# Performance work log

Hardware: AMD Instinct MI355X
Metric: run time of the kernel (lower is better)

The kernel has to match this reference:

```python
import jax, jax.numpy as jnp
import numpy as np

N_SUB, N_AGR, N_URB = 200000, 400000, 200000
H, OUT = 64, 6
E_SS, E_AS, E_US = 2000000, 4000000, 2000000
NLAYERS = 3


def setup_inputs() -> dict:
    key = jax.random.key(0)
    ks = jax.random.split(key, 12)
    s = 0.05
    return {
        "x_sub": jax.random.normal(ks[0], (N_SUB, H), jnp.float32),
        "x_agr": jax.random.normal(ks[1], (N_AGR, H), jnp.float32),
        "x_urb": jax.random.normal(ks[2], (N_URB, H), jnp.float32),
        # stacked SAGEConv params: [layer, relation(ss,as,us), ...]
        "Wl": jax.random.normal(ks[3], (NLAYERS, 3, H, H), jnp.float32) * s,
        "bl": jax.random.normal(ks[4], (NLAYERS, 3, H), jnp.float32) * s,
        "Wr": jax.random.normal(ks[5], (NLAYERS, 3, H, H), jnp.float32) * s,
        "Wf": jax.random.normal(ks[6], (OUT, H), jnp.float32) * s,
        "bf": jnp.zeros((OUT,), jnp.float32),
        "edge_ss": jax.random.randint(ks[7], (2, E_SS), 0, N_SUB, jnp.int32),
        "edge_as_src": jax.random.randint(ks[8], (E_AS,), 0, N_AGR, jnp.int32),
        "edge_as_dst": jax.random.randint(ks[9], (E_AS,), 0, N_SUB, jnp.int32),
        "edge_us": jax.random.randint(ks[10], (2, E_US), 0, N_SUB, jnp.int32),
    }


def _sage(x_src, x_dst, src, dst, Wl, b, Wr, n_dst, mean):
    # PyG SAGEConv: lin_l(aggr_j x_j) + lin_r(x_i); lin_r has no bias
    msg = x_src[src]                                   # [E, d_src] gather
    agg = jax.ops.segment_sum(msg, dst, num_segments=n_dst)
    if mean:  # static python flag
        deg = jax.ops.segment_sum(jnp.ones((src.shape[0], 1), x_src.dtype),
                                  dst, num_segments=n_dst)
        agg = agg / jnp.maximum(deg, 1.0)
    return agg @ Wl.T + b + x_dst @ Wr.T


def reference(x_sub, x_agr, x_urb, Wl, bl, Wr, Wf, bf,
              edge_ss, edge_as_src, edge_as_dst, edge_us):
    sub = x_sub
    for i in range(NLAYERS):
        mean_ss = i > 0  # layer-0 sub->sub uses aggr='sum', later layers PyG default 'mean'
        h = _sage(sub, sub, edge_ss[0], edge_ss[1], Wl[i, 0], bl[i, 0], Wr[i, 0], N_SUB, mean_ss)
        h = h + _sage(x_agr, sub, edge_as_src, edge_as_dst, Wl[i, 1], bl[i, 1], Wr[i, 1], N_SUB, False)
        h = h + _sage(x_urb, sub, edge_us[0], edge_us[1], Wl[i, 2], bl[i, 2], Wr[i, 2], N_SUB, False)
        sub = jax.nn.relu(h)  # Identity norm (batch_norm=False), dropout is eval-mode identity
        # x_dict['agr'] / x_dict['urb'] reset to skip features -> agr/urb convs never affect output
    return jax.nn.softmax(sub @ Wf.T + bf, axis=1)
```

## Files before the change

### kernel.cpp

```cpp
#include <hip/hip_runtime.h>
#include <cstdio>
#include <cstdint>


#define NSUB 200000
#define NAGR 400000
#define NURB 200000
#define HDIM 64
#define ESS 2000000
#define EAS 4000000
#define EUS 2000000
#define NB 512
#define CAP_AS 8608
#define CAP_SS 4320
#define CAP_US 4320
#define CHUNK 4096
#define NCH_AS 977
#define NCH_SS 489
#define NCH_US 489
#define COL_SLACK 16384
#define CDIV(a,b) (((a)+(b)-1)/(b))

using u16 = unsigned short;
typedef __attribute__((ext_vector_type(8))) short v8s;
typedef __attribute__((ext_vector_type(4))) float v4f;
typedef __attribute__((ext_vector_type(2))) float v2f;
typedef __attribute__((ext_vector_type(4))) unsigned int v4u;

__device__ __forceinline__ float bu2f(u16 u){
  union { unsigned int i; float f; } c; c.i = ((unsigned int)u) << 16; return c.f;
}
__device__ __forceinline__ u16 f2bu(float x){
  union { float f; unsigned int i; } c; c.f = x;
  unsigned int r = c.i + 0x7fffu + ((c.i >> 16) & 1u);
  return (u16)(r >> 16);
}
__device__ __forceinline__ int bucket_of(int d){
  return (int)(((unsigned long long)(unsigned)d * NB) / NSUB);
}
__device__ __forceinline__ int bucket_base(int b){
  return (int)(((unsigned long long)b * NSUB + NB - 1) / NB);
}

__global__ void kcast(const float4* __restrict__ in, uint2* __restrict__ outp, int n4){
  int i = blockIdx.x*256 + threadIdx.x;
  if(i<n4){
    float4 v = in[i];
    uint2 o;
    o.x = (unsigned int)f2bu(v.x) | ((unsigned int)f2bu(v.y)<<16);
    o.y = (unsigned int)f2bu(v.z) | ((unsigned int)f2bu(v.w)<<16);
    outp[i]=o;
  }
}

__global__ void kcast2(const float4* __restrict__ a, uint2* __restrict__ oa, int n4a,
                       const float4* __restrict__ u, uint2* __restrict__ ou, int n4u){
  int i = blockIdx.x*256 + threadIdx.x;
  if(i < n4a){
    float4 v = a[i];
    uint2 o;
    o.x = (unsigned int)f2bu(v.x) | ((unsigned int)f2bu(v.y)<<16);
    o.y = (unsigned int)f2bu(v.z) | ((unsigned int)f2bu(v.w)<<16);
    oa[i]=o;
  } else if(i < n4a + n4u){
    int idx = i - n4a;
    float4 v = u[idx];
    uint2 o;
    o.x = (unsigned int)f2bu(v.x) | ((unsigned int)f2bu(v.y)<<16);
    o.y = (unsigned int)f2bu(v.z) | ((unsigned int)f2bu(v.w)<<16);
    ou[idx]=o;
  } else {
    int k = i - n4a - n4u;
    uint2 z; z.x=0u; z.y=0u;
    if(k < 16) oa[(size_t)n4a + k] = z;
    else if(k < 32) ou[(size_t)n4u + (k-16)] = z;
  }
}

__global__ void kprep(const float* __restrict__ Wl, const float* __restrict__ Wr,
                      const float* __restrict__ bl, u16* __restrict__ Wg,
                      float* __restrict__ bsum, int* __restrict__ gcur,
                      u16* __restrict__ zA, u16* __restrict__ zB){
  int l = blockIdx.x, tid = threadIdx.x;
  for(int i=tid; i<16384; i+=256){
    int o = i>>8, k = i&255, a = k>>6, kk = k&63;
    float v;
    if(a<3) v = Wl[(((size_t)l*3+a)*64+o)*64+kk];
    else    v = Wr[(((size_t)l*3+0)*64+o)*64+kk]
              + Wr[(((size_t)l*3+1)*64+o)*64+kk]
              + Wr[(((size_t)l*3+2)*64+o)*64+kk];
    Wg[((size_t)l*64+o)*256 + k] = f2bu(v);
  }
  if(tid<64) bsum[l*64+tid] = bl[(l*3+0)*64+tid] + bl[(l*3+1)*64+tid] + bl[(l*3+2)*64+tid];
  for(int i=tid;i<NB;i+=256) gcur[l*NB+i]=0;
  if(l==0){
    uint2 z; z.x=0u; z.y=0u;
    if(tid<16)          ((uint2*)(zA + (size_t)NSUB*HDIM))[tid]    = z;
    else if(tid<32)     ((uint2*)(zB + (size_t)NSUB*HDIM))[tid-16] = z;
  }
}

__global__ __launch_bounds__(256) void kpart(
    const int* __restrict__ e_ss, const int* __restrict__ e_as_s,
    const int* __restrict__ e_as_d, const int* __restrict__ e_us,
    unsigned* __restrict__ pAS, unsigned* __restrict__ pSS,
    unsigned* __restrict__ pUS, int* __restrict__ gcur){
  __shared__ int cnt[NB];
  __shared__ int seg[NB];
  int bid = blockIdx.x, tid = threadIdx.x;
  int rel, chunk, cap, Erel;
  const int *sp, *dp; unsigned* part;
  if(bid < NCH_AS){ rel=0; chunk=bid; sp=e_as_s; dp=e_as_d; part=pAS; cap=CAP_AS; Erel=EAS; }
  else if(bid < NCH_AS+NCH_SS){ rel=1; chunk=bid-NCH_AS; sp=e_ss; dp=e_ss+ESS; part=pSS; cap=CAP_SS; Erel=ESS; }
  else { rel=2; chunk=bid-NCH_AS-NCH_SS; sp=e_us; dp=e_us+EUS; part=pUS; cap=CAP_US; Erel=EUS; }
  int m = Erel - chunk*CHUNK; if(m>CHUNK) m=CHUNK;
  for(int i=tid;i<NB;i+=256) cnt[i]=0;
  __syncthreads();
  unsigned pk[16], meta[16];
  #pragma unroll
  for(int j=0;j<16;j++){
    int idx = j*256+tid;
    meta[j] = 0xFFFFFFFFu;
    if(idx < m){
      long i = (long)chunk*CHUNK + idx;
      int s = sp[i], d = dp[i];
      int b = bucket_of(d);
      int r = atomicAdd(&cnt[b],1);
      pk[j] = ((unsigned)s<<9) | (unsigned)(d - bucket_base(b));
      meta[j] = ((unsigned)b<<16) | (unsigned)r;
    }
  }
  __syncthreads();
  for(int q=tid;q<NB;q+=256){
    int c = cnt[q];
    seg[q] = c ? atomicAdd(&gcur[rel*NB+q], c) : 0;
  }
  __syncthreads();
  #pragma unroll
  for(int j=0;j<16;j++){
    if(meta[j]!=0xFFFFFFFFu){
      int b = meta[j]>>16, r = meta[j]&0xFFFF;
      int pos = seg[b] + r;
      if(pos < cap) part[(long)b*cap + pos] = pk[j];
    }
  }
}

__global__ void kbscan(const int* __restrict__ gcur, int* __restrict__ boff){
  __shared__ int s1[256];
  int t = threadIdx.x;
  for(int rel=0; rel<3; rel++){
    int cap = (rel==0)?CAP_AS:((rel==1)?CAP_SS:CAP_US);
    int g0 = gcur[rel*NB + 2*t], g1 = gcur[rel*NB + 2*t+1];
    int a0 = g0<cap?g0:cap, a1 = g1<cap?g1:cap;
    s1[t] = a0+a1;
    __syncthreads();
    for(int off=1; off<256; off<<=1){
      int x = s1[t];
      int y = (t>=off)?s1[t-off]:0;
      __syncthreads();
      s1[t] = x+y;
      __syncthreads();
    }
    int e2 = s1[t]-(a0+a1);
    boff[rel*NB + 2*t]   = e2;
    boff[rel*NB + 2*t+1] = e2+a0;
    __syncthreads();
  }
}

__global__ __launch_bounds__(256) void ksort(
    const unsigned* __restrict__ pAS, const unsigned* __restrict__ pSS,
    const unsigned* __restrict__ pUS, const int* __restrict__ gcur,
    const int* __restrict__ boff,
    int* __restrict__ colAS, int* __restrict__ colSS, int* __restrict__ colUS,
    int* __restrict__ rpAS, int* __restrict__ rpSS, int* __restrict__ rpUS,
    int* __restrict__ degAS, int* __restrict__ degSS, int* __restrict__ degUS){
  __shared__ int degl[512];
  __shared__ int excl[512];
  __shared__ int cur[512];
  __shared__ int s1[256];
  int bid = blockIdx.x;
  int rel = bid >> 9, b = bid & 511;
  const unsigned* part; int cap; int* col; int* rp; int* deg;
  if(rel==0){ part=pAS; cap=CAP_AS; col=colAS; rp=rpAS; deg=degAS; }
  else if(rel==1){ part=pSS; cap=CAP_SS; col=colSS; rp=rpSS; deg=degSS; }
  else { part=pUS; cap=CAP_US; col=colUS; rp=rpUS; deg=degUS; }
  int tid = threadIdx.x;
  int base_b = bucket_base(b);
  int base_n = (b+1==NB)?NSUB:bucket_base(b+1);
  int width = base_n - base_b;
  int size = gcur[rel*NB+b]; if(size>cap) size=cap;
  int bo = boff[rel*NB+b];
  const unsigned* pb = part + (long)b*cap;
  degl[tid]=0; degl[256+tid]=0;
  __syncthreads();
  for(int i=tid;i<size;i+=256) atomicAdd(&degl[pb[i]&511u],1);
  __syncthreads();
  int a0=degl[2*tid], a1=degl[2*tid+1];
  s1[tid]=a0+a1;
  __syncthreads();
  for(int off=1; off<256; off<<=1){
    int x=s1[tid];
    int y=(tid>=off)?s1[tid-off]:0;
    __syncthreads();
    s1[tid]=x+y;
    __syncthreads();
  }
  int e2 = s1[tid]-(a0+a1);
  excl[2*tid]=e2;     excl[2*tid+1]=e2+a0;
  cur[2*tid]=e2;      cur[2*tid+1]=e2+a0;
  __syncthreads();
  for(int n=tid;n<width;n+=256){
    rp[base_b+n]  = bo + excl[n];
    deg[base_b+n] = degl[n];
  }
  for(int i=tid;i<size;i+=256){
    unsigned p = pb[i];
    int dl = (int)(p&511u);
    int r = atomicAdd(&cur[dl],1);
    col[bo + r] = (int)(p>>9);
  }
}

__device__ __forceinline__ float gather1(const float* x, size_t idx){ return x[idx]; }

template<bool MEAN>
__device__ __forceinline__ void agg_one_f32(const float* __restrict__ x,
    const int* __restrict__ rowptr, const int* __restrict__ deg,
    const int* __restrict__ col, u16* __restrict__ out, int w, int lane){
  int s = __builtin_amdgcn_readfirstlane(rowptr[w]);
  int d = __builtin_amdgcn_readfirstlane(deg[w]);
  float acc = 0.f;
  int i=0;
  for(; i+8<=d; i+=8){
    int sj[8];
    #pragma unroll
    for(int j=0;j<8;j++) sj[j]=col[s+i+j];
    float a[8];
    #pragma unroll
    for(int j=0;j<8;j++) a[j]=gather1(x,(size_t)sj[j]*HDIM+lane);
    acc += ((a[0]+a[1])+(a[2]+a[3])) + ((a[4]+a[5])+(a[6]+a[7]));
  }
  for(; i<d; i++) acc += gather1(x,(size_t)col[s+i]*HDIM+lane);
  float sc = 1.f;
  if(MEAN) sc = 1.f/(float)(d>1?d:1);
  out[(size_t)w*HDIM + lane] = f2bu(acc*sc);
}

__global__ __launch_bounds__(256) void kaggAUf(
    const float* __restrict__ xa, const int* __restrict__ rpA,
    const int* __restrict__ degA, const int* __restrict__ colA,
    u16* __restrict__ outA,
    const float* __restrict__ xu, const int* __restrict__ rpU,
    const int* __restrict__ degU, const int* __restrict__ colU,
    u16* __restrict__ outU){
  int gid = blockIdx.x*256 + threadIdx.x;
  int w = gid>>6, lane = gid&63;
  if(w < NSUB)        agg_one_f32<false>(xa, rpA, degA, colA, outA, w, lane);
  else if(w < 2*NSUB) agg_one_f32<false>(xu, rpU, degU, colU, outU, w-NSUB, lane);
}

template<bool MEAN>
__device__ __forceinline__ void agg_pair(const u16* __restrict__ x,
    const int* __restrict__ rowptr, const int* __restrict__ deg,
    const int* __restrict__ col, u16* __restrict__ out,
    int w0, int lane, int zrow){
  int h  = lane>>5;
  int gl = (lane>>3)&3;
  int q  = lane&7;
  int w  = w0 + h;
  int s  = rowptr[w];
  int d  = deg[w];
  int d0 = __builtin_amdgcn_readlane(d, 0);
  int d1 = __builtin_amdgcn_readlane(d, 32);
  int dm = d0 > d1 ? d0 : d1;
  const u16* xq = x + ((unsigned)q<<3);
  v2f acc[4];
  #pragma unroll
  for(int k=0;k<4;k++){ acc[k].x=0.f; acc[k].y=0.f; }
  for(int i=0; i<dm; i+=16){
    int eb = i + gl;
    const int* cp = col + (s + eb);
    int cj[4];
    #pragma unroll
    for(int j=0;j<4;j++){
      int c = cp[j*4];
      cj[j] = (eb + j*4 < d) ? c : zrow;
    }
    v8s vv[4];
    #pragma unroll
    for(int j=0;j<4;j++)
      vv[j] = *(const v8s*)(xq + (size_t)(unsigned)cj[j]*HDIM);
    #pragma unroll
    for(int j=0;j<4;j++){
      v4u dw = __builtin_bit_cast(v4u, vv[j]);
      #pragma unroll
      for(int k=0;k<4;k++){
        unsigned v = dw[k];
        v2f p;
        p.x = __uint_as_float(v << 16);
        p.y = __uint_as_float(v & 0xffff0000u);
        acc[k] += p;
      }
    }
  }
  #pragma unroll
  for(int k=0;k<4;k++){
    v2f v = acc[k];
    v2f t;
    t.x = __shfl_xor(v.x, 8);  t.y = __shfl_xor(v.y, 8);  v += t;
    t.x = __shfl_xor(v.x, 16); t.y = __shfl_xor(v.y, 16); v += t;
    acc[k] = v;
  }
  float sc = 1.f;
  if(MEAN) sc = 1.f/(float)(d>1?d:1);
  if(gl==0){
    v4u r;
    #pragma unroll
    for(int k=0;k<4;k++)
      r[k] = (unsigned)f2bu(acc[k].x*sc) | ((unsigned)f2bu(acc[k].y*sc)<<16);
    *(v4u*)(out + (size_t)w*HDIM + ((unsigned)q<<3)) = r;
  }
}

template<bool MEAN>
__global__ __launch_bounds__(256) void kaggP(
    const u16* __restrict__ x, const int* __restrict__ rowptr,
    const int* __restrict__ deg, const int* __restrict__ col,
    u16* __restrict__ out, int npair, int zrow){
  int gid = blockIdx.x*256 + threadIdx.x;
  int p = gid>>6, lane = gid&63;
  if(p>=npair) return;
  agg_pair<MEAN>(x, rowptr, deg, col, out, 2*p, lane, zrow);
}

__global__ __launch_bounds__(256) void kaggAUP(
    const u16* __restrict__ xa, const int* __restrict__ rpA,
    const int* __restrict__ degA, const int* __restrict__ colA,
    u16* __restrict__ outA,
    const u16* __restrict__ xu, const int* __restrict__ rpU,
    const int* __restrict__ degU, const int* __restrict__ colU,
    u16* __restrict__ outU){
  int gid = blockIdx.x*256 + threadIdx.x;
  int p = gid>>6, lane = gid&63;
  if(p < NSUB/2)      agg_pair<false>(xa, rpA, degA, colA, outA, 2*p, lane, NAGR);
  else if(p < NSUB)   agg_pair<false>(xu, rpU, degU, colU, outU, 2*(p-NSUB/2), lane, NURB);
}

__global__ __launch_bounds__(256) void kgemmM(
    const u16* __restrict__ aggSS, const u16* __restrict__ aggAS,
    const u16* __restrict__ aggUS, const u16* __restrict__ subIn,
    const u16* __restrict__ Wg, const float* __restrict__ bsum,
    u16* __restrict__ subOut){
  __shared__ u16 ldsW[64*264];
  __shared__ float ldsB[64];
  int tid = threadIdx.x;
  const unsigned* wg32 = (const unsigned*)Wg;
  for(int i=tid; i<8192; i+=256){
    int o = i>>7, k2 = i&127;
    ((unsigned*)ldsW)[o*132 + k2] = wg32[i];
  }
  if(tid<64) ldsB[tid] = bsum[tid];
  __syncthreads();
  int lane = tid&63, wid = tid>>6;
  long row0 = (long)blockIdx.x*64 + wid*16;
  const u16* arrs[4] = {aggSS, aggAS, aggUS, subIn};
  v4f acc[4] = {};
  long rowl = row0 + (lane&15);
  int kq = (lane>>4)*8;
  #pragma unroll
  for(int s=0;s<8;s++){
    const u16* ap = arrs[s>>1] + rowl*64 + (s&1)*32 + kq;
    v8s a = *(const v8s*)ap;
    #pragma unroll
    for(int t=0;t<4;t++){
      v8s bf = *(const v8s*)&ldsW[(t*16+(lane&15))*264 + s*32 + kq];
      acc[t] = __builtin_amdgcn_mfma_f32_16x16x32_bf16(a, bf, acc[t], 0,0,0);
    }
  }
  int m0 = (lane>>4)*4;
  #pragma unroll
  for(int t=0;t<4;t++){
    int o = t*16 + (lane&15);
    float bb = ldsB[o];
    #pragma unroll
    for(int r=0;r<4;r++){
      float h = acc[t][r] + bb;
      h = fmaxf(h, 0.f);
      subOut[(row0 + m0 + r)*64 + o] = f2bu(h);
    }
  }
}

__global__ void khead(const u16* __restrict__ sub, const float* __restrict__ Wf,
                      const float* __restrict__ bfv, float* __restrict__ out, int n){
  __shared__ float w[6*64];
  __shared__ float b[6];
  for(int j=threadIdx.x; j<384; j+=256) w[j]=Wf[j];
  if(threadIdx.x<6) b[threadIdx.x]=bfv[threadIdx.x];
  __syncthreads();
  int i = blockIdx.x*256 + threadIdx.x;
  if(i>=n) return;
  const unsigned int* row = (const unsigned int*)(sub + (size_t)i*HDIM);
  float d0=b[0],d1=b[1],d2=b[2],d3=b[3],d4=b[4],d5=b[5];
  #pragma unroll 8
  for(int k2=0;k2<32;k2++){
    unsigned int v = row[k2];
    float lo = bu2f((u16)(v&0xffffu));
    float hi = bu2f((u16)(v>>16));
    int k = 2*k2;
    d0 += lo*w[0*64+k] + hi*w[0*64+k+1];
    d1 += lo*w[1*64+k] + hi*w[1*64+k+1];
    d2 += lo*w[2*64+k] + hi*w[2*64+k+1];
    d3 += lo*w[3*64+k] + hi*w[3*64+k+1];
    d4 += lo*w[4*64+k] + hi*w[4*64+k+1];
    d5 += lo*w[5*64+k] + hi*w[5*64+k+1];
  }
  float m = fmaxf(fmaxf(fmaxf(d0,d1),fmaxf(d2,d3)),fmaxf(d4,d5));
  float e0=expf(d0-m), e1=expf(d1-m), e2=expf(d2-m);
  float e3=expf(d3-m), e4=expf(d4-m), e5=expf(d5-m);
  float inv = 1.0f/(e0+e1+e2+e3+e4+e5);
  float2* op = (float2*)(out + (size_t)i*6);
  float2 r0; r0.x=e0*inv; r0.y=e1*inv;
  float2 r1; r1.x=e2*inv; r1.y=e3*inv;
  float2 r2; r2.x=e4*inv; r2.y=e5*inv;
  op[0]=r0; op[1]=r1; op[2]=r2;
}

extern "C" void kernel_launch(void* const* d_in, const int* in_sizes, int n_in,
                              void* d_out, int out_size, void* d_ws, size_t ws_size,
                              hipStream_t stream) {
  const float* x_sub = (const float*)d_in[0];
  const float* x_agr = (const float*)d_in[1];
  const float* x_urb = (const float*)d_in[2];
  const float* Wl    = (const float*)d_in[3];
  const float* bl    = (const float*)d_in[4];
  const float* Wr    = (const float*)d_in[5];
  const float* Wf    = (const float*)d_in[6];
  const float* bfv   = (const float*)d_in[7];
  const int* e_ss    = (const int*)d_in[8];
  const int* e_as_s  = (const int*)d_in[9];
  const int* e_as_d  = (const int*)d_in[10];
  const int* e_us    = (const int*)d_in[11];
  float* out = (float*)d_out;

  char* ws = (char*)d_ws;
  size_t off = 0;
  auto alloc = [&](size_t bytes)->void*{
    void* p = ws + off; off += (bytes + 255) & ~(size_t)255; return p;
  };
  u16*  subA   = (u16*) alloc((size_t)(NSUB+1)*HDIM*2);
  u16*  subB   = (u16*) alloc((size_t)(NSUB+1)*HDIM*2);
  u16*  aggSS  = (u16*) alloc((size_t)NSUB*HDIM*2);
  u16*  aggAS  = (u16*) alloc((size_t)NSUB*HDIM*2);
  u16*  aggUS  = (u16*) alloc((size_t)NSUB*HDIM*2);
  int*  colAS  = (int*)  alloc((size_t)(EAS+COL_SLACK)*4);
  int*  colSS  = (int*)  alloc((size_t)(ESS+COL_SLACK)*4);
  int*  colUS  = (int*)  alloc((size_t)(EUS+COL_SLACK)*4);
  int*  rpAS   = (int*)  alloc((size_t)NSUB*4);
  int*  rpSS   = (int*)  alloc((size_t)NSUB*4);
  int*  rpUS   = (int*)  alloc((size_t)NSUB*4);
  int*  degAS  = (int*)  alloc((size_t)NSUB*4);
  int*  degSS  = (int*)  alloc((size_t)NSUB*4);
  int*  degUS  = (int*)  alloc((size_t)NSUB*4);
  int*  gcur   = (int*)  alloc((size_t)3*NB*4);
  int*  boff   = (int*)  alloc((size_t)3*NB*4);
  u16*  Wg     = (u16*)  alloc((size_t)3*64*256*2);
  float* bsum  = (float*)alloc((size_t)3*64*4);
  size_t off0 = off;
  unsigned* pAS = (unsigned*)alloc((size_t)NB*CAP_AS*4);
  unsigned* pSS = (unsigned*)alloc((size_t)NB*CAP_SS*4);
  unsigned* pUS = (unsigned*)alloc((size_t)NB*CAP_US*4);
  size_t end_part = off;
  u16* agr16 = (u16*)(ws + off0);
  u16* urb16 = agr16 + (size_t)(NAGR+1)*HDIM;
  size_t end_cast = off0 + ((size_t)NAGR+NURB+2)*HDIM*2;
  size_t need_full = end_part > end_cast ? end_part : end_cast;
  bool bf16_gather = (ws_size >= need_full);
  if(ws_size < end_part){
    fprintf(stderr, "kernel_launch: ws too small: need %zu have %zu\n", end_part, ws_size);
    return;
  }

  kcast<<<CDIV(NSUB*HDIM/4,256),256,0,stream>>>((const float4*)x_sub, (uint2*)subA, NSUB*HDIM/4);
  kprep<<<3,256,0,stream>>>(Wl, Wr, bl, Wg, bsum, gcur, subA, subB);

  kpart<<<NCH_AS+NCH_SS+NCH_US,256,0,stream>>>(e_ss, e_as_s, e_as_d, e_us,
                                               pAS, pSS, pUS, gcur);
  kbscan<<<1,256,0,stream>>>(gcur, boff);
  ksort<<<3*NB,256,0,stream>>>(pAS, pSS, pUS, gcur, boff,
                               colAS, colSS, colUS,
                               rpAS, rpSS, rpUS,
                               degAS, degSS, degUS);

  if(bf16_gather){
    int n4a = NAGR*HDIM/4, n4u = NURB*HDIM/4;
    kcast2<<<CDIV(n4a+n4u+32,256),256,0,stream>>>((const float4*)x_agr, (uint2*)agr16, n4a,
                                                  (const float4*)x_urb, (uint2*)urb16, n4u);
    kaggAUP<<<NSUB*64/256,256,0,stream>>>(agr16, rpAS, degAS, colAS, aggAS,
                                          urb16, rpUS, degUS, colUS, aggUS);
  } else {
    kaggAUf<<<CDIV(2*NSUB*64,256),256,0,stream>>>(x_agr, rpAS, degAS, colAS, aggAS,
                                                  x_urb, rpUS, degUS, colUS, aggUS);
  }

  const int pairBlocks = (NSUB/2)*64/256;
  const int gemmBlocks = NSUB/64;
  kaggP<false><<<pairBlocks,256,0,stream>>>(subA, rpSS, degSS, colSS, aggSS, NSUB/2, NSUB);
  kgemmM<<<gemmBlocks,256,0,stream>>>(aggSS, aggAS, aggUS, subA, Wg + 0*16384, bsum + 0*64, subB);
  kaggP<true><<<pairBlocks,256,0,stream>>>(subB, rpSS, degSS, colSS, aggSS, NSUB/2, NSUB);
  kgemmM<<<gemmBlocks,256,0,stream>>>(aggSS, aggAS, aggUS, subB, Wg + 1*16384, bsum + 1*64, subA);
  kaggP<true><<<pairBlocks,256,0,stream>>>(subA, rpSS, degSS, colSS, aggSS, NSUB/2, NSUB);
  kgemmM<<<gemmBlocks,256,0,stream>>>(aggSS, aggAS, aggUS, subA, Wg + 2*16384, bsum + 2*64, subB);

  khead<<<CDIV(NSUB,256),256,0,stream>>>(subB, Wf, bfv, out, NSUB);
}
```

Before: 756.8 us.

## Pad CSR rows to multiples of four, pack rowptr/deg, vectorize column loads

```diff
diff --git a/kernel.cpp b/kernel.cpp
--- a/kernel.cpp
+++ b/kernel.cpp
@@ -18,7 +18,7 @@
 #define NCH_AS 977
 #define NCH_SS 489
 #define NCH_US 489
-#define COL_SLACK 16384
+#define COL_PAD (4*NSUB + 256)
 #define CDIV(a,b) (((a)+(b)-1)/(b))
 
 using u16 = unsigned short;
@@ -151,8 +151,11 @@
   int t = threadIdx.x;
   for(int rel=0; rel<3; rel++){
     int cap = (rel==0)?CAP_AS:((rel==1)?CAP_SS:CAP_US);
-    int g0 = gcur[rel*NB + 2*t], g1 = gcur[rel*NB + 2*t+1];
-    int a0 = g0<cap?g0:cap, a1 = g1<cap?g1:cap;
+    int n0 = 2*t, n1 = 2*t+1;
+    int w0 = bucket_base(n0+1) - bucket_base(n0);
+    int w1 = bucket_base(n1+1) - bucket_base(n1);
+    int g0 = gcur[rel*NB + n0], g1 = gcur[rel*NB + n1];
+    int a0 = (g0<cap?g0:cap) + 4*w0, a1 = (g1<cap?g1:cap) + 4*w1;
     s1[t] = a0+a1;
     __syncthreads();
     for(int off=1; off<256; off<<=1){
@@ -163,8 +166,8 @@
       __syncthreads();
     }
     int e2 = s1[t]-(a0+a1);
-    boff[rel*NB + 2*t]   = e2;
-    boff[rel*NB + 2*t+1] = e2+a0;
+    boff[rel*NB + n0] = e2;
+    boff[rel*NB + n1] = e2+a0;
     __syncthreads();
   }
 }
@@ -174,18 +177,17 @@
     const unsigned* __restrict__ pUS, const int* __restrict__ gcur,
     const int* __restrict__ boff,
     int* __restrict__ colAS, int* __restrict__ colSS, int* __restrict__ colUS,
-    int* __restrict__ rpAS, int* __restrict__ rpSS, int* __restrict__ rpUS,
-    int* __restrict__ degAS, int* __restrict__ degSS, int* __restrict__ degUS){
+    int2* __restrict__ rpdAS, int2* __restrict__ rpdSS, int2* __restrict__ rpdUS){
   __shared__ int degl[512];
   __shared__ int excl[512];
   __shared__ int cur[512];
   __shared__ int s1[256];
   int bid = blockIdx.x;
   int rel = bid >> 9, b = bid & 511;
-  const unsigned* part; int cap; int* col; int* rp; int* deg;
-  if(rel==0){ part=pAS; cap=CAP_AS; col=colAS; rp=rpAS; deg=degAS; }
-  else if(rel==1){ part=pSS; cap=CAP_SS; col=colSS; rp=rpSS; deg=degSS; }
-  else { part=pUS; cap=CAP_US; col=colUS; rp=rpUS; deg=degUS; }
+  const unsigned* part; int cap; int* col; int2* rpd;
+  if(rel==0){ part=pAS; cap=CAP_AS; col=colAS; rpd=rpdAS; }
+  else if(rel==1){ part=pSS; cap=CAP_SS; col=colSS; rpd=rpdSS; }
+  else { part=pUS; cap=CAP_US; col=colUS; rpd=rpdUS; }
   int tid = threadIdx.x;
   int base_b = bucket_base(b);
   int base_n = (b+1==NB)?NSUB:bucket_base(b+1);
@@ -197,7 +199,7 @@
   __syncthreads();
   for(int i=tid;i<size;i+=256) atomicAdd(&degl[pb[i]&511u],1);
   __syncthreads();
-  int a0=degl[2*tid], a1=degl[2*tid+1];
+  int a0=(degl[2*tid]+3)&~3, a1=(degl[2*tid+1]+3)&~3;
   s1[tid]=a0+a1;
   __syncthreads();
   for(int off=1; off<256; off<<=1){
@@ -212,8 +214,8 @@
   cur[2*tid]=e2;      cur[2*tid+1]=e2+a0;
   __syncthreads();
   for(int n=tid;n<width;n+=256){
-    rp[base_b+n]  = bo + excl[n];
-    deg[base_b+n] = degl[n];
+    int2 v; v.x = bo + excl[n]; v.y = degl[n];
+    rpd[base_b+n] = v;
   }
   for(int i=tid;i<size;i+=256){
     unsigned p = pb[i];
@@ -223,14 +225,13 @@
   }
 }
 
-__device__ __forceinline__ float gather1(const float* x, size_t idx){ return x[idx]; }
-
 template<bool MEAN>
 __device__ __forceinline__ void agg_one_f32(const float* __restrict__ x,
-    const int* __restrict__ rowptr, const int* __restrict__ deg,
+    const int2* __restrict__ rpd,
     const int* __restrict__ col, u16* __restrict__ out, int w, int lane){
-  int s = __builtin_amdgcn_readfirstlane(rowptr[w]);
-  int d = __builtin_amdgcn_readfirstlane(deg[w]);
+  int2 rd = rpd[w];
+  int s = __builtin_amdgcn_readfirstlane(rd.x);
+  int d = __builtin_amdgcn_readfirstlane(rd.y);
   float acc = 0.f;
   int i=0;
   for(; i+8<=d; i+=8){
@@ -239,39 +240,49 @@
     for(int j=0;j<8;j++) sj[j]=col[s+i+j];
     float a[8];
     #pragma unroll
-    for(int j=0;j<8;j++) a[j]=gather1(x,(size_t)sj[j]*HDIM+lane);
+    for(int j=0;j<8;j++) a[j]=x[(size_t)sj[j]*HDIM+lane];
     acc += ((a[0]+a[1])+(a[2]+a[3])) + ((a[4]+a[5])+(a[6]+a[7]));
   }
-  for(; i<d; i++) acc += gather1(x,(size_t)col[s+i]*HDIM+lane);
+  for(; i<d; i++) acc += x[(size_t)col[s+i]*HDIM+lane];
   float sc = 1.f;
   if(MEAN) sc = 1.f/(float)(d>1?d:1);
   out[(size_t)w*HDIM + lane] = f2bu(acc*sc);
 }
 
 __global__ __launch_bounds__(256) void kaggAUf(
-    const float* __restrict__ xa, const int* __restrict__ rpA,
-    const int* __restrict__ degA, const int* __restrict__ colA,
-    u16* __restrict__ outA,
-    const float* __restrict__ xu, const int* __restrict__ rpU,
-    const int* __restrict__ degU, const int* __restrict__ colU,
-    u16* __restrict__ outU){
+    const float* __restrict__ xa, const int2* __restrict__ rpdA,
+    const int* __restrict__ colA, u16* __restrict__ outA,
+    const float* __restrict__ xu, const int2* __restrict__ rpdU,
+    const int* __restrict__ colU, u16* __restrict__ outU){
   int gid = blockIdx.x*256 + threadIdx.x;
   int w = gid>>6, lane = gid&63;
-  if(w < NSUB)        agg_one_f32<false>(xa, rpA, degA, colA, outA, w, lane);
-  else if(w < 2*NSUB) agg_one_f32<false>(xu, rpU, degU, colU, outU, w-NSUB, lane);
+  if(w < NSUB)        agg_one_f32<false>(xa, rpdA, colA, outA, w, lane);
+  else if(w < 2*NSUB) agg_one_f32<false>(xu, rpdU, colU, outU, w-NSUB, lane);
+}
+
+__device__ __forceinline__ void unpack_acc(v8s vvj, v2f acc[4]){
+  v4u dw = __builtin_bit_cast(v4u, vvj);
+  #pragma unroll
+  for(int k=0;k<4;k++){
+    unsigned v = dw[k];
+    v2f p;
+    p.x = __uint_as_float(v << 16);
+    p.y = __uint_as_float(v & 0xffff0000u);
+    acc[k] += p;
+  }
 }
 
 template<bool MEAN>
 __device__ __forceinline__ void agg_pair(const u16* __restrict__ x,
-    const int* __restrict__ rowptr, const int* __restrict__ deg,
+    const int2* __restrict__ rpd,
     const int* __restrict__ col, u16* __restrict__ out,
     int w0, int lane, int zrow){
   int h  = lane>>5;
   int gl = (lane>>3)&3;
   int q  = lane&7;
   int w  = w0 + h;
-  int s  = rowptr[w];
-  int d  = deg[w];
+  int2 rd = rpd[w];
+  int s = rd.x, d = rd.y;
   int d0 = __builtin_amdgcn_readlane(d, 0);
   int d1 = __builtin_amdgcn_readlane(d, 32);
   int dm = d0 > d1 ? d0 : d1;
@@ -279,30 +290,34 @@
   v2f acc[4];
   #pragma unroll
   for(int k=0;k<4;k++){ acc[k].x=0.f; acc[k].y=0.f; }
-  for(int i=0; i<dm; i+=16){
-    int eb = i + gl;
-    const int* cp = col + (s + eb);
-    int cj[4];
-    #pragma unroll
-    for(int j=0;j<4;j++){
-      int c = cp[j*4];
-      cj[j] = (eb + j*4 < d) ? c : zrow;
-    }
+  if(dm <= 16){
+    const int4 c4 = *(const int4*)(col + s + 4*gl);
+    int cj[4] = {c4.x, c4.y, c4.z, c4.w};
+    #pragma unroll
+    for(int j=0;j<4;j++) cj[j] = (4*gl + j < d) ? cj[j] : zrow;
     v8s vv[4];
     #pragma unroll
     for(int j=0;j<4;j++)
       vv[j] = *(const v8s*)(xq + (size_t)(unsigned)cj[j]*HDIM);
     #pragma unroll
-    for(int j=0;j<4;j++){
-      v4u dw = __builtin_bit_cast(v4u, vv[j]);
+    for(int j=0;j<4;j++) unpack_acc(vv[j], acc);
+  } else {
+    for(int i=0; i<dm; i+=32){
+      const int4 cA = *(const int4*)(col + s + i + 4*gl);
+      const int4 cB = *(const int4*)(col + s + i + 16 + 4*gl);
+      int cj[8] = {cA.x,cA.y,cA.z,cA.w, cB.x,cB.y,cB.z,cB.w};
+      int eb = i + 4*gl;
       #pragma unroll
-      for(int k=0;k<4;k++){
-        unsigned v = dw[k];
-        v2f p;
-        p.x = __uint_as_float(v << 16);
-        p.y = __uint_as_float(v & 0xffff0000u);
-        acc[k] += p;
+      for(int j=0;j<8;j++){
+        int e = eb + (j&3) + ((j>>2)<<4);
+        cj[j] = (e < d) ? cj[j] : zrow;
       }
+      v8s vv[8];
+      #pragma unroll
+      for(int j=0;j<8;j++)
+        vv[j] = *(const v8s*)(xq + (size_t)(unsigned)cj[j]*HDIM);
+      #pragma unroll
+      for(int j=0;j<8;j++) unpack_acc(vv[j], acc);
     }
   }
   #pragma unroll
@@ -326,26 +341,24 @@
 
 template<bool MEAN>
 __global__ __launch_bounds__(256) void kaggP(
-    const u16* __restrict__ x, const int* __restrict__ rowptr,
-    const int* __restrict__ deg, const int* __restrict__ col,
+    const u16* __restrict__ x, const int2* __restrict__ rpd,
+    const int* __restrict__ col,
     u16* __restrict__ out, int npair, int zrow){
   int gid = blockIdx.x*256 + threadIdx.x;
   int p = gid>>6, lane = gid&63;
   if(p>=npair) return;
-  agg_pair<MEAN>(x, rowptr, deg, col, out, 2*p, lane, zrow);
+  agg_pair<MEAN>(x, rpd, col, out, 2*p, lane, zrow);
 }
 
 __global__ __launch_bounds__(256) void kaggAUP(
-    const u16* __restrict__ xa, const int* __restrict__ rpA,
-    const int* __restrict__ degA, const int* __restrict__ colA,
-    u16* __restrict__ outA,
-    const u16* __restrict__ xu, const int* __restrict__ rpU,
-    const int* __restrict__ degU, const int* __restrict__ colU,
-    u16* __restrict__ outU){
+    const u16* __restrict__ xa, const int2* __restrict__ rpdA,
+    const int* __restrict__ colA, u16* __restrict__ outA,
+    const u16* __restrict__ xu, const int2* __restrict__ rpdU,
+    const int* __restrict__ colU, u16* __restrict__ outU){
   int gid = blockIdx.x*256 + threadIdx.x;
   int p = gid>>6, lane = gid&63;
-  if(p < NSUB/2)      agg_pair<false>(xa, rpA, degA, colA, outA, 2*p, lane, NAGR);
-  else if(p < NSUB)   agg_pair<false>(xu, rpU, degU, colU, outU, 2*(p-NSUB/2), lane, NURB);
+  if(p < NSUB/2)      agg_pair<false>(xa, rpdA, colA, outA, 2*p, lane, NAGR);
+  else if(p < NSUB)   agg_pair<false>(xu, rpdU, colU, outU, 2*(p-NSUB/2), lane, NURB);
 }
 
 __global__ __launch_bounds__(256) void kgemmM(
@@ -455,15 +468,12 @@
   u16*  aggSS  = (u16*) alloc((size_t)NSUB*HDIM*2);
   u16*  aggAS  = (u16*) alloc((size_t)NSUB*HDIM*2);
   u16*  aggUS  = (u16*) alloc((size_t)NSUB*HDIM*2);
-  int*  colAS  = (int*)  alloc((size_t)(EAS+COL_SLACK)*4);
-  int*  colSS  = (int*)  alloc((size_t)(ESS+COL_SLACK)*4);
-  int*  colUS  = (int*)  alloc((size_t)(EUS+COL_SLACK)*4);
-  int*  rpAS   = (int*)  alloc((size_t)NSUB*4);
-  int*  rpSS   = (int*)  alloc((size_t)NSUB*4);
-  int*  rpUS   = (int*)  alloc((size_t)NSUB*4);
-  int*  degAS  = (int*)  alloc((size_t)NSUB*4);
-  int*  degSS  = (int*)  alloc((size_t)NSUB*4);
-  int*  degUS  = (int*)  alloc((size_t)NSUB*4);
+  int*  colAS  = (int*)  alloc((size_t)(EAS+COL_PAD)*4);
+  int*  colSS  = (int*)  alloc((size_t)(ESS+COL_PAD)*4);
+  int*  colUS  = (int*)  alloc((size_t)(EUS+COL_PAD)*4);
+  int2* rpdAS  = (int2*) alloc((size_t)NSUB*8);
+  int2* rpdSS  = (int2*) alloc((size_t)NSUB*8);
+  int2* rpdUS  = (int2*) alloc((size_t)NSUB*8);
   int*  gcur   = (int*)  alloc((size_t)3*NB*4);
   int*  boff   = (int*)  alloc((size_t)3*NB*4);
   u16*  Wg     = (u16*)  alloc((size_t)3*64*256*2);
@@ -491,27 +501,26 @@
   kbscan<<<1,256,0,stream>>>(gcur, boff);
   ksort<<<3*NB,256,0,stream>>>(pAS, pSS, pUS, gcur, boff,
                                colAS, colSS, colUS,
-                               rpAS, rpSS, rpUS,
-                               degAS, degSS, degUS);
+                               rpdAS, rpdSS, rpdUS);
 
   if(bf16_gather){
     int n4a = NAGR*HDIM/4, n4u = NURB*HDIM/4;
     kcast2<<<CDIV(n4a+n4u+32,256),256,0,stream>>>((const float4*)x_agr, (uint2*)agr16, n4a,
                                                   (const float4*)x_urb, (uint2*)urb16, n4u);
-    kaggAUP<<<NSUB*64/256,256,0,stream>>>(agr16, rpAS, degAS, colAS, aggAS,
-                                          urb16, rpUS, degUS, colUS, aggUS);
+    kaggAUP<<<NSUB*64/256,256,0,stream>>>(agr16, rpdAS, colAS, aggAS,
+                                          urb16, rpdUS, colUS, aggUS);
   } else {
-    kaggAUf<<<CDIV(2*NSUB*64,256),256,0,stream>>>(x_agr, rpAS, degAS, colAS, aggAS,
-                                                  x_urb, rpUS, degUS, colUS, aggUS);
+    kaggAUf<<<CDIV(2*NSUB*64,256),256,0,stream>>>(x_agr, rpdAS, colAS, aggAS,
+                                                  x_urb, rpdUS, colUS, aggUS);
   }
 
   const int pairBlocks = (NSUB/2)*64/256;
   const int gemmBlocks = NSUB/64;
-  kaggP<false><<<pairBlocks,256,0,stream>>>(subA, rpSS, degSS, colSS, aggSS, NSUB/2, NSUB);
+  kaggP<false><<<pairBlocks,256,0,stream>>>(subA, rpdSS, colSS, aggSS, NSUB/2, NSUB);
   kgemmM<<<gemmBlocks,256,0,stream>>>(aggSS, aggAS, aggUS, subA, Wg + 0*16384, bsum + 0*64, subB);
-  kaggP<true><<<pairBlocks,256,0,stream>>>(subB, rpSS, degSS, colSS, aggSS, NSUB/2, NSUB);
+  kaggP<true><<<pairBlocks,256,0,stream>>>(subB, rpdSS, colSS, aggSS, NSUB/2, NSUB);
   kgemmM<<<gemmBlocks,256,0,stream>>>(aggSS, aggAS, aggUS, subB, Wg + 1*16384, bsum + 1*64, subA);
-  kaggP<true><<<pairBlocks,256,0,stream>>>(subA, rpSS, degSS, colSS, aggSS, NSUB/2, NSUB);
+  kaggP<true><<<pairBlocks,256,0,stream>>>(subA, rpdSS, colSS, aggSS, NSUB/2, NSUB);
   kgemmM<<<gemmBlocks,256,0,stream>>>(aggSS, aggAS, aggUS, subA, Wg + 2*16384, bsum + 2*64, subB);
 
   khead<<<CDIV(NSUB,256),256,0,stream>>>(subB, Wf, bfv, out, NSUB);
```

Result: slower. 789.6 us (+4.3%).
